# Performance work log

Hardware: AMD Instinct MI355X
Metric: run time of the kernel (lower is better)

Reference implementation:

```python
import jax, jax.numpy as jnp
import numpy as np

NUME = 100000
H, DH, K, R = 4, 32, 16, 17
DIN, DT, DOUT = 128, 32, 128
N0, N1, N2 = 131072, 32768, 4096
B, HIST = 2048, 2
LN_EPS = 1e-5


def setup_inputs() -> dict:
    key = jax.random.key(0)
    ks = jax.random.split(key, 16)
    din = DIN + DT
    inp = {}
    inp["emb"] = jax.random.normal(ks[0], (NUME, DIN), jnp.float32) * 0.1
    inp["freq"] = jnp.asarray(1.0 / 10 ** np.linspace(0, 9, DT), jnp.float32)
    inp["phase"] = jnp.zeros((DT,), jnp.float32)
    for l in (0, 1):
        inp[f"gamma{l}"] = jnp.ones((din,), jnp.float32)
        inp[f"beta{l}"] = jnp.zeros((din,), jnp.float32)
        inp[f"W{l}"] = jax.random.normal(ks[1 + 5 * l], (R, din, H * DH), jnp.float32) * 0.05
        inp[f"attn_l{l}"] = jax.random.normal(ks[2 + 5 * l], (R, H, DH), jnp.float32) * 0.05
        inp[f"attn_r{l}"] = jax.random.normal(ks[3 + 5 * l], (R, H, DH), jnp.float32) * 0.05
        inp[f"bias{l}"] = jnp.zeros((R, H * DH), jnp.float32)
    inp["src_ids0"] = jax.random.randint(ks[11], (N0,), 0, NUME * 100)
    inp["src_idx0"] = jax.random.randint(ks[12], (R, N1, K), 0, N0)
    inp["src_ids1"] = jax.random.randint(ks[13], (N1,), 0, NUME * 100)
    inp["src_idx1"] = jax.random.randint(ks[14], (R, N2, K), 0, N1)
    inp["root_idx"] = jax.random.randint(ks[15], (B * HIST,), 0, N2)
    inp["ts"] = 99
    return inp


def _gat_layer(h, src_ids, src_idx, gamma, beta, W, al, ar, b, ts, freq, phase):
    # h: [Nsrc, din-DT] src-node features; src_idx: [R, Ndst, K] neighbor ids.
    ndst = src_idx.shape[1]
    # TimeEnc: cos((ts - nid // nume) * freq + phase)
    t = (ts - src_ids // NUME).astype(h.dtype)
    phi = jnp.cos(t[:, None] * freq + phase)  # [Nsrc, DT]
    h = jnp.concatenate([h, phi], axis=1)
    # LayerNorm
    mu = jnp.mean(h, axis=-1, keepdims=True)
    var = jnp.mean((h - mu) ** 2, axis=-1, keepdims=True)
    h = (h - mu) * jax.lax.rsqrt(var + LN_EPS) * gamma + beta

    def body(acc, xs):
        Wr, alr, arr, br, idx = xs
        proj = (h @ Wr).reshape(-1, H, DH)               # [Nsrc, H, DH]
        el = jnp.einsum('nhe,he->nh', proj, alr)         # [Nsrc, H]
        er = jnp.einsum('nhe,he->nh', proj[:ndst], arr)  # [Ndst, H]
        e = jax.nn.leaky_relu(el[idx] + er[:, None, :], 0.2)  # [Ndst, K, H]
        a = jax.nn.softmax(e, axis=1)                    # edge softmax over K
        out = jnp.einsum('ikh,ikhe->ihe', a, proj[idx]) + br.reshape(H, DH)
        return acc + out, None

    acc, _ = jax.lax.scan(body, jnp.zeros((ndst, H, DH), h.dtype),
                          (W, al, ar, b, src_idx))
    # HeteroGraphConv aggregate='mean' over R relation outputs, then ReLU
    return jax.nn.relu((acc / R).reshape(ndst, H * DH))


def reference(emb, freq, phase,
              gamma0, beta0, W0, attn_l0, attn_r0, bias0,
              gamma1, beta1, W1, attn_l1, attn_r1, bias1,
              src_ids0, src_idx0, src_ids1, src_idx1, root_idx, ts):
    h = emb[src_ids0 % NUME]  # entity embedding lookup [N0, DIN]
    h = _gat_layer(h, src_ids0, src_idx0, gamma0, beta0, W0, attn_l0, attn_r0,
                   bias0, ts, freq, phase)
    h = _gat_layer(h, src_ids1, src_idx1, gamma1, beta1, W1, attn_l1, attn_r1,
                   bias1, ts, freq, phase)
    # gather root embeddings and fold hist dimension into features
    return h[root_idx].reshape(B, HIST * DOUT)
```

## Files before the change

### kernel.cpp

```cpp
#include <hip/hip_runtime.h>
#include <hip/hip_bf16.h>

#define NUME 100000
constexpr int H      = 4;
constexpr int DH     = 32;
constexpr int KNB    = 16;
constexpr int R      = 17;
constexpr int DIN    = 128;
constexpr int DT     = 32;
constexpr int DINT   = 160;
constexpr int N0     = 131072;
constexpr int N1     = 32768;
constexpr int N2     = 4096;
constexpr float LN_EPS = 1e-5f;

typedef unsigned short ushort_t;
typedef ushort_t us2 __attribute__((ext_vector_type(2)));
typedef ushort_t us8 __attribute__((ext_vector_type(8)));
typedef short    s8v __attribute__((ext_vector_type(8)));
typedef float    f32x4 __attribute__((ext_vector_type(4)));

__device__ __forceinline__ float bf2f(ushort_t u) {
    return __uint_as_float(((unsigned int)u) << 16);
}
__device__ __forceinline__ ushort_t f2bf(float f) {
    unsigned int x = __float_as_uint(f);
    unsigned int r = x + 0x7fffu + ((x >> 16) & 1u);
    return (ushort_t)(r >> 16);
}

__global__ __launch_bounds__(256) void k_wcast(
    const float* __restrict__ W, ushort_t* __restrict__ wt, int total)
{
    int t = blockIdx.x * blockDim.x + threadIdx.x;
    if (t >= total) return;
    int r   = t / (DINT * DIN);
    int rem = t % (DINT * DIN);
    int k   = rem >> 7;
    int n   = rem & 127;
    wt[(size_t)r * DIN * DINT + (size_t)n * DINT + k] = f2bf(W[t]);
}

__global__ __launch_bounds__(256) void k_prep(
    const float* __restrict__ srcf,
    const int*   __restrict__ ids,
    const int*   __restrict__ ts_ptr,
    const float* __restrict__ freq,
    const float* __restrict__ phase,
    const float* __restrict__ gamma,
    const float* __restrict__ beta,
    ushort_t*    __restrict__ hn,
    int n_rows, int mode)
{
    int wid  = (int)((blockIdx.x * blockDim.x + threadIdx.x) >> 6);
    int lane = threadIdx.x & 63;
    if (wid >= n_rows) return;

    int id = ids[wid];
    const float* row = (mode == 1)
        ? (srcf + (size_t)(id % NUME) * DIN)
        : (srcf + (size_t)wid * DIN);

    float x0 = row[lane];
    float x1 = row[lane + 64];
    if (mode == 0) {
        x0 = fmaxf(x0 * (1.f / (float)R), 0.f);
        x1 = fmaxf(x1 * (1.f / (float)R), 0.f);
    }

    int   ts = ts_ptr[0];
    float t  = (float)(ts - id / NUME);
    float p  = 0.f;
    if (lane < DT) p = cosf(t * freq[lane] + phase[lane]);

    float s  = x0 + x1 + p;
    float sq = x0*x0 + x1*x1 + p*p;
    #pragma unroll
    for (int m = 1; m < 64; m <<= 1) {
        s  += __shfl_xor(s,  m);
        sq += __shfl_xor(sq, m);
    }
    float mu   = s / (float)DINT;
    float var  = sq / (float)DINT - mu * mu;
    float rstd = rsqrtf(var + LN_EPS);

    size_t base = (size_t)wid * DINT;
    hn[base + lane]      = f2bf((x0 - mu) * rstd * gamma[lane]      + beta[lane]);
    hn[base + 64 + lane] = f2bf((x1 - mu) * rstd * gamma[64 + lane] + beta[64 + lane]);
    if (lane < DT)
        hn[base + 128 + lane] = f2bf((p - mu) * rstd * gamma[128 + lane] + beta[128 + lane]);
}

__global__ __launch_bounds__(256) void k_gemm(
    const ushort_t* __restrict__ A,
    const ushort_t* __restrict__ Bt,
    const float*    __restrict__ al,
    const float*    __restrict__ ar,
    ushort_t*       __restrict__ C,
    float*          __restrict__ el,
    float*          __restrict__ er,
    int ndst)
{
    __shared__ ushort_t As[128][40];
    __shared__ ushort_t Bs[128][40];

    int tid  = threadIdx.x;
    int lane = tid & 63;
    int wave = tid >> 6;
    int wr   = wave >> 1;
    int wc   = wave & 1;
    int row0 = blockIdx.x * 128;

    f32x4 acc[4][4];
    #pragma unroll
    for (int i = 0; i < 4; ++i)
        #pragma unroll
        for (int j = 0; j < 4; ++j) acc[i][j] = (f32x4){0.f, 0.f, 0.f, 0.f};

    for (int kc = 0; kc < DINT; kc += 32) {
        #pragma unroll
        for (int j = 0; j < 2; ++j) {
            int f  = tid + j * 256;
            int m  = f >> 2;
            int ko = (f & 3) * 8;
            *(us8*)&As[m][ko] = *(const us8*)&A [(size_t)(row0 + m) * DINT + kc + ko];
            *(us8*)&Bs[m][ko] = *(const us8*)&Bt[(size_t)m          * DINT + kc + ko];
        }
        __syncthreads();

        s8v af[4], bfr[4];
        #pragma unroll
        for (int i = 0; i < 4; ++i)
            af[i] = *(const s8v*)&As[wr*64 + i*16 + (lane & 15)][(lane >> 4) * 8];
        #pragma unroll
        for (int j = 0; j < 4; ++j)
            bfr[j] = *(const s8v*)&Bs[wc*64 + j*16 + (lane & 15)][(lane >> 4) * 8];

        #pragma unroll
        for (int i = 0; i < 4; ++i)
            #pragma unroll
            for (int j = 0; j < 4; ++j)
                acc[i][j] = __builtin_amdgcn_mfma_f32_16x16x32_bf16(
                                af[i], bfr[j], acc[i][j], 0, 0, 0);
        __syncthreads();
    }

    #pragma unroll
    for (int i = 0; i < 4; ++i) {
        #pragma unroll
        for (int j = 0; j < 4; ++j) {
            int col  = wc*64 + j*16 + (lane & 15);
            int rowb = row0 + wr*64 + i*16 + ((lane >> 4) << 2);
            #pragma unroll
            for (int q = 0; q < 4; ++q)
                C[(size_t)(rowb + q) * DIN + col] = f2bf(acc[i][j][q]);
        }
    }

    float alv[4], arv[4];
    #pragma unroll
    for (int j = 0; j < 4; ++j) {
        int c = wc*64 + j*16 + (lane & 15);
        alv[j] = al[c];
        arv[j] = ar[c];
    }
    int b0 = lane & 1;
    int b1 = (lane >> 1) & 1;
    #pragma unroll
    for (int i = 0; i < 4; ++i) {
        #pragma unroll
        for (int q = 0; q < 4; ++q) {
            float pl0 = acc[i][0][q]*alv[0] + acc[i][1][q]*alv[1];
            float pl1 = acc[i][2][q]*alv[2] + acc[i][3][q]*alv[3];
            float pr0 = acc[i][0][q]*arv[0] + acc[i][1][q]*arv[1];
            float pr1 = acc[i][2][q]*arv[2] + acc[i][3][q]*arv[3];
            float t;
            t = __shfl_xor(b0 ? pl0 : pl1, 1);
            float vA = (b0 ? pl1 : pl0) + t;
            t = __shfl_xor(b0 ? pr0 : pr1, 1);
            float vB = (b0 ? pr1 : pr0) + t;
            t = __shfl_xor(b1 ? vA : vB, 2);
            float vC = (b1 ? vB : vA) + t;
            vC += __shfl_xor(vC, 4);
            vC += __shfl_xor(vC, 8);
            if ((lane & 12) == 0) {
                int row = row0 + wr*64 + i*16 + ((lane >> 4) << 2) + q;
                int h   = 2*wc + b0;
                if (!b1) {
                    el[(size_t)row * 4 + h] = vC;
                } else if (row < ndst) {
                    er[(size_t)row * 4 + h] = vC;
                }
            }
        }
    }
}

__global__ __launch_bounds__(256) void k_agg(
    const ushort_t* __restrict__ proj,
    const int*      __restrict__ idx,
    const float*    __restrict__ el,
    const float*    __restrict__ er,
    const float*    __restrict__ br,
    float*          __restrict__ accg,
    int ndst)
{
    int wid  = (int)((blockIdx.x * blockDim.x + threadIdx.x) >> 6);
    if (wid >= ndst) return;
    int l = threadIdx.x & 63;

    int jv = idx[(size_t)wid * KNB + (l & 15)];

    int   jk = __shfl(jv, l >> 2);
    float e  = el[(size_t)jk * 4 + (l & 3)] + er[(size_t)wid * 4 + (l & 3)];
    e = e > 0.f ? e : 0.2f * e;
    float mx = e;
    #pragma unroll
    for (int m = 4; m < 64; m <<= 1) mx = fmaxf(mx, __shfl_xor(mx, m));
    float p = __expf(e - mx);
    float s = p;
    #pragma unroll
    for (int m = 4; m < 64; m <<= 1) s += __shfl_xor(s, m);
    float a = p / s;

    int rsub = l >> 4;
    int fg   = l & 15;
    float vacc[8];
    #pragma unroll
    for (int t = 0; t < 8; ++t) vacc[t] = 0.f;

    #pragma unroll
    for (int kk = 0; kk < 4; ++kk) {
        int   j  = __shfl(jv, 4*kk + rsub);
        float ak = __shfl(a, 16*kk + 4*rsub + (fg >> 2));
        us8   v  = *(const us8*)&proj[(size_t)j * DIN + fg * 8];
        #pragma unroll
        for (int t = 0; t < 8; ++t) vacc[t] = fmaf(ak, bf2f(v[t]), vacc[t]);
    }
    #pragma unroll
    for (int t = 0; t < 8; ++t) {
        vacc[t] += __shfl_xor(vacc[t], 16);
        vacc[t] += __shfl_xor(vacc[t], 32);
    }
    if (l < 16) {
        float* ap = accg + (size_t)wid * DIN + l * 8;
        #pragma unroll
        for (int t = 0; t < 8; ++t) ap[t] += vacc[t] + br[l * 8 + t];
    }
}

__global__ __launch_bounds__(256) void k_root(
    const float* __restrict__ acc, const int* __restrict__ root,
    float* __restrict__ out, int n)
{
    int t = blockIdx.x * blockDim.x + threadIdx.x;
    if (t < n) {
        float x = acc[(size_t)root[t >> 7] * DIN + (t & 127)];
        out[t] = fmaxf(x * (1.f / (float)R), 0.f);
    }
}

extern "C" void kernel_launch(void* const* d_in, const int* in_sizes, int n_in,
                              void* d_out, int out_size, void* d_ws, size_t ws_size,
                              hipStream_t stream)
{
    const float* emb    = (const float*)d_in[0];
    const float* freq   = (const float*)d_in[1];
    const float* phase  = (const float*)d_in[2];
    const float* gamma0 = (const float*)d_in[3];
    const float* beta0  = (const float*)d_in[4];
    const float* W0     = (const float*)d_in[5];
    const float* al0    = (const float*)d_in[6];
    const float* ar0    = (const float*)d_in[7];
    const float* b0     = (const float*)d_in[8];
    const float* gamma1 = (const float*)d_in[9];
    const float* beta1  = (const float*)d_in[10];
    const float* W1     = (const float*)d_in[11];
    const float* al1    = (const float*)d_in[12];
    const float* ar1    = (const float*)d_in[13];
    const float* b1     = (const float*)d_in[14];
    const int* src_ids0 = (const int*)d_in[15];
    const int* src_idx0 = (const int*)d_in[16];
    const int* src_ids1 = (const int*)d_in[17];
    const int* src_idx1 = (const int*)d_in[18];
    const int* root     = (const int*)d_in[19];
    const int* ts       = (const int*)d_in[20];
    float* out = (float*)d_out;

    ushort_t* hn   = (ushort_t*)d_ws;
    ushort_t* proj = hn   + (size_t)N0 * DINT;
    float*    acc  = (float*)(proj + (size_t)N0 * DIN);
    float*    el   = acc  + (size_t)N1 * DIN;
    float*    er   = el   + (size_t)N0 * 4;
    ushort_t* wt0  = (ushort_t*)(er + (size_t)N1 * 4);
    ushort_t* wt1  = wt0 + (size_t)R * DIN * DINT;

    const int WTOT = R * DINT * DIN;

    k_wcast<<<(WTOT + 255) / 256, 256, 0, stream>>>(W0, wt0, WTOT);
    hipMemsetAsync(acc, 0, (size_t)N1 * DIN * sizeof(float), stream);
    k_prep<<<N0 / 4, 256, 0, stream>>>(emb, src_ids0, ts, freq, phase,
                                       gamma0, beta0, hn, N0, 1);
    for (int r = 0; r < R; ++r) {
        k_gemm<<<N0 / 128, 256, 0, stream>>>(hn, wt0 + (size_t)r * DIN * DINT,
                                             al0 + r * 128, ar0 + r * 128,
                                             proj, el, er, N1);
        k_agg<<<N1 / 4, 256, 0, stream>>>(proj,
                                          src_idx0 + (size_t)r * N1 * KNB,
                                          el, er, b0 + r * 128, acc, N1);
    }

    k_wcast<<<(WTOT + 255) / 256, 256, 0, stream>>>(W1, wt1, WTOT);
    k_prep<<<N1 / 4, 256, 0, stream>>>(acc, src_ids1, ts, freq, phase,
                                       gamma1, beta1, hn, N1, 0);
    hipMemsetAsync(acc, 0, (size_t)N2 * DIN * sizeof(float), stream);
    for (int r = 0; r < R; ++r) {
        k_gemm<<<N1 / 128, 256, 0, stream>>>(hn, wt1 + (size_t)r * DIN * DINT,
                                             al1 + r * 128, ar1 + r * 128,
                                             proj, el, er, N2);
        k_agg<<<N2 / 4, 256, 0, stream>>>(proj,
                                          src_idx1 + (size_t)r * N2 * KNB,
                                          el, er, b1 + r * 128, acc, N2);
    }

    k_root<<<(N2 * DIN) / 256, 256, 0, stream>>>(acc, root, out, N2 * DIN);
}
```

Before: 1.449 ms.

## Double-buffer A tiles and preload full B into registers in projection GEMM

The projection GEMM kernel now loads the whole B (weight) matrix into shared memory once and keeps all five K-slices of B fragments in registers. A tiles are double-buffered: the next K-chunk is prefetched from global memory into registers while the current MFMAs run, then written to the alternate LDS buffer. This removes one of the two barriers per K step and overlaps global loads with compute. The cost is more LDS (a 128x168 B tile) and much higher register pressure (the 20 B fragments), which could reduce occupancy.

Result: no change. 1.447 ms (-0.1%).

```diff
diff --git a/kernel.cpp b/kernel.cpp
--- a/kernel.cpp
+++ b/kernel.cpp
@@ -101,8 +101,8 @@
     float*          __restrict__ er,
     int ndst)
 {
-    __shared__ ushort_t As[128][40];
-    __shared__ ushort_t Bs[128][40];
+    __shared__ ushort_t Bs[128][168];
+    __shared__ ushort_t As[2][128][40];
 
     int tid  = threadIdx.x;
     int lane = tid & 63;
@@ -111,37 +111,66 @@
     int wc   = wave & 1;
     int row0 = blockIdx.x * 128;
 
-    f32x4 acc[4][4];
-    #pragma unroll
-    for (int i = 0; i < 4; ++i)
-        #pragma unroll
-        for (int j = 0; j < 4; ++j) acc[i][j] = (f32x4){0.f, 0.f, 0.f, 0.f};
-
-    for (int kc = 0; kc < DINT; kc += 32) {
+    {
+        int bm  = tid >> 1;
+        int bko = (tid & 1) * 80;
+        #pragma unroll
+        for (int g = 0; g < 10; ++g)
+            *(us8*)&Bs[bm][bko + g * 8] =
+                *(const us8*)&Bt[(size_t)bm * DINT + bko + g * 8];
         #pragma unroll
         for (int j = 0; j < 2; ++j) {
             int f  = tid + j * 256;
             int m  = f >> 2;
             int ko = (f & 3) * 8;
-            *(us8*)&As[m][ko] = *(const us8*)&A [(size_t)(row0 + m) * DINT + kc + ko];
-            *(us8*)&Bs[m][ko] = *(const us8*)&Bt[(size_t)m          * DINT + kc + ko];
-        }
-        __syncthreads();
-
-        s8v af[4], bfr[4];
+            *(us8*)&As[0][m][ko] = *(const us8*)&A[(size_t)(row0 + m) * DINT + ko];
+        }
+    }
+    __syncthreads();
+
+    s8v breg[5][4];
+    #pragma unroll
+    for (int kk = 0; kk < 5; ++kk)
+        #pragma unroll
+        for (int j = 0; j < 4; ++j)
+            breg[kk][j] = *(const s8v*)&Bs[wc*64 + j*16 + (lane & 15)]
+                                          [kk*32 + (lane >> 4) * 8];
+
+    f32x4 acc[4][4];
+    #pragma unroll
+    for (int i = 0; i < 4; ++i)
+        #pragma unroll
+        for (int j = 0; j < 4; ++j) acc[i][j] = (f32x4){0.f, 0.f, 0.f, 0.f};
+
+    #pragma unroll
+    for (int kc = 0; kc < 5; ++kc) {
+        us8 pa[2];
+        int m0 = 0, ko0 = 0, m1 = 0, ko1 = 0;
+        if (kc < 4) {
+            int f0 = tid;
+            m0  = f0 >> 2; ko0 = (f0 & 3) * 8;
+            pa[0] = *(const us8*)&A[(size_t)(row0 + m0) * DINT + (kc + 1) * 32 + ko0];
+            int f1 = tid + 256;
+            m1  = f1 >> 2; ko1 = (f1 & 3) * 8;
+            pa[1] = *(const us8*)&A[(size_t)(row0 + m1) * DINT + (kc + 1) * 32 + ko1];
+        }
+
+        s8v af[4];
         #pragma unroll
         for (int i = 0; i < 4; ++i)
-            af[i] = *(const s8v*)&As[wr*64 + i*16 + (lane & 15)][(lane >> 4) * 8];
-        #pragma unroll
-        for (int j = 0; j < 4; ++j)
-            bfr[j] = *(const s8v*)&Bs[wc*64 + j*16 + (lane & 15)][(lane >> 4) * 8];
-
+            af[i] = *(const s8v*)&As[kc & 1][wr*64 + i*16 + (lane & 15)]
+                                            [(lane >> 4) * 8];
         #pragma unroll
         for (int i = 0; i < 4; ++i)
             #pragma unroll
             for (int j = 0; j < 4; ++j)
                 acc[i][j] = __builtin_amdgcn_mfma_f32_16x16x32_bf16(
-                                af[i], bfr[j], acc[i][j], 0, 0, 0);
+                                af[i], breg[kc][j], acc[i][j], 0, 0, 0);
+
+        if (kc < 4) {
+            *(us8*)&As[(kc + 1) & 1][m0][ko0] = pa[0];
+            *(us8*)&As[(kc + 1) & 1][m1][ko1] = pa[1];
+        }
         __syncthreads();
     }
 
```
